# Optimization experiments

Measured on AMD Instinct MI355X. Metric: run time of the kernel, lower is better.

The kernel has to match this reference:

```python
import jax, jax.numpy as jnp
import numpy as np

B, S, D_IN, D_OUT, H = 4, 2048, 1024, 1024, 16
HD = D_OUT // H  # head_dim = 64


def setup_inputs() -> dict:
    key = jax.random.key(0)
    ks = jax.random.split(key, 7)
    sd_in = 1.0 / np.sqrt(D_IN)
    sd_out = 1.0 / np.sqrt(D_OUT)
    return {
        "x": jax.random.normal(ks[0], (B, S, D_IN), dtype=jnp.float32),
        # weights stored [in, out] so y = x @ W (equivalent to torch Linear)
        "wq": jax.random.uniform(ks[1], (D_IN, D_OUT), jnp.float32, -sd_in, sd_in),
        "wk": jax.random.uniform(ks[2], (D_IN, D_OUT), jnp.float32, -sd_in, sd_in),
        "wv": jax.random.uniform(ks[3], (D_IN, D_OUT), jnp.float32, -sd_in, sd_in),
        "wo": jax.random.uniform(ks[4], (D_OUT, D_OUT), jnp.float32, -sd_out, sd_out),
        "bo": jax.random.uniform(ks[5], (D_OUT,), jnp.float32, -sd_out, sd_out),
    }


def reference(x, wq, wk, wv, wo, bo):
    b, n, _ = x.shape
    # project and split heads: [b, h, n, hd]
    q = (x @ wq).reshape(b, n, H, HD).transpose(0, 2, 1, 3)
    k = (x @ wk).reshape(b, n, H, HD).transpose(0, 2, 1, 3)
    v = (x @ wv).reshape(b, n, H, HD).transpose(0, 2, 1, 3)
    scale = 1.0 / jnp.sqrt(jnp.asarray(HD, dtype=x.dtype))
    scores = jnp.einsum('bhqd,bhkd->bhqk', q, k) * scale  # [b,h,n,n]
    causal = jnp.tril(jnp.ones((n, n), dtype=bool))
    scores = jnp.where(causal, scores, -jnp.inf)
    attn = jax.nn.softmax(scores, axis=-1)
    # dropout p=0.0 -> identity
    ctx = jnp.einsum('bhqk,bhkd->bhqd', attn, v)
    ctx = ctx.transpose(0, 2, 1, 3).reshape(b, n, D_OUT)
    return ctx @ wo + bo
```

## Files before the change

kernel.cpp:

```cpp
#include <hip/hip_runtime.h>

#define DEVINL __device__ __forceinline__

typedef __attribute__((ext_vector_type(8))) short s8v;
typedef __attribute__((ext_vector_type(4))) float f4v;
typedef __attribute__((ext_vector_type(16))) float f16v;
typedef __attribute__((ext_vector_type(8))) __bf16 bf8v;
typedef __attribute__((ext_vector_type(4))) unsigned int u4v;

static constexpr int SEQ = 2048;
static constexpr int DIM = 1024;
static constexpr int NH = 16;

DEVINL unsigned short f2bf(float f) {
  unsigned int u = __builtin_bit_cast(unsigned int, f);
  u += 0x7FFFu + ((u >> 16) & 1u);
  return (unsigned short)(u >> 16);
}

DEVINL void gl_lds16(const void* g, void* l) {
  __builtin_amdgcn_global_load_lds((__attribute__((address_space(1))) void*)g,
                                   (__attribute__((address_space(3))) void*)l,
                                   16, 0, 0);
}

DEVINL f4v mfma16(s8v a, s8v b, f4v c) {
  return __builtin_amdgcn_mfma_f32_16x16x32_bf16(__builtin_bit_cast(bf8v, a),
                                                 __builtin_bit_cast(bf8v, b),
                                                 c, 0, 0, 0);
}

DEVINL f16v mfma32(s8v a, s8v b, f16v c) {
  return __builtin_amdgcn_mfma_f32_32x32x16_bf16(__builtin_bit_cast(bf8v, a),
                                                 __builtin_bit_cast(bf8v, b),
                                                 c, 0, 0, 0);
}

DEVINL unsigned cvtpk(float lo, float hi) {
  unsigned r;
  asm("v_cvt_pk_bf16_f32 %0, %1, %2" : "=v"(r) : "v"(lo), "v"(hi));
  return r;
}

DEVINL void plswap(unsigned& a, unsigned& b) {
#if __has_builtin(__builtin_amdgcn_permlane32_swap)
  typedef int i2v __attribute__((ext_vector_type(2)));
  i2v r = __builtin_amdgcn_permlane32_swap((int)a, (int)b, false, false);
  a = (unsigned)r[0]; b = (unsigned)r[1];
#else
  asm volatile("v_permlane32_swap_b32 %0, %1" : "+v"(a), "+v"(b));
#endif
}

DEVINL s8v mkfrag(unsigned w0, unsigned w1, unsigned w2, unsigned w3) {
  u4v t = {w0, w1, w2, w3};
  return __builtin_bit_cast(s8v, t);
}

__global__ __launch_bounds__(256) void k_cvt(const float* __restrict__ in,
                                             unsigned short* __restrict__ outp) {
  const int i = blockIdx.x * 256 + threadIdx.x;
  const f4v* p = (const f4v*)in + (size_t)i * 2;
  f4v a = p[0], b = p[1];
  s8v o;
  o[0] = (short)f2bf(a[0]); o[1] = (short)f2bf(a[1]);
  o[2] = (short)f2bf(a[2]); o[3] = (short)f2bf(a[3]);
  o[4] = (short)f2bf(b[0]); o[5] = (short)f2bf(b[1]);
  o[6] = (short)f2bf(b[2]); o[7] = (short)f2bf(b[3]);
  ((s8v*)outp)[i] = o;
}

__global__ __launch_bounds__(256) void k_twt(const float* __restrict__ w0, const float* __restrict__ w1,
                                             const float* __restrict__ w2, const float* __restrict__ w3,
                                             unsigned short* __restrict__ o0, unsigned short* __restrict__ o1,
                                             unsigned short* __restrict__ o2, unsigned short* __restrict__ o3) {
  __shared__ float tile[32][33];
  const float* w = blockIdx.z == 0 ? w0 : blockIdx.z == 1 ? w1 : blockIdx.z == 2 ? w2 : w3;
  unsigned short* o = blockIdx.z == 0 ? o0 : blockIdx.z == 1 ? o1 : blockIdx.z == 2 ? o2 : o3;
  const int r0 = blockIdx.y * 32, c0 = blockIdx.x * 32;
  const int tx = threadIdx.x & 31, ty = threadIdx.x >> 5;
#pragma unroll
  for (int i = 0; i < 32; i += 8) tile[ty + i][tx] = w[(r0 + ty + i) * DIM + c0 + tx];
  __syncthreads();
#pragma unroll
  for (int i = 0; i < 32; i += 8) o[(c0 + ty + i) * DIM + r0 + tx] = f2bf(tile[tx][ty + i]);
}

static constexpr int SLOT = 49152;
static constexpr int RING_LDS = 147456;

DEVINL void stage_ab(const unsigned short* __restrict__ A, const unsigned short* __restrict__ Bt,
                     int m0, int n0, int k0, char* slot, int tid) {
#pragma unroll
  for (int ld = 0; ld < 2; ++ld) {
    const int c = ld * 512 + tid;
    const int row = c >> 3;
    const int csw = ((c & 7) ^ (row & 7)) * 8;
    gl_lds16(A + (size_t)(m0 + row) * 1024 + k0 + csw, slot + c * 16);
  }
#pragma unroll
  for (int ld = 0; ld < 4; ++ld) {
    const int c = ld * 512 + tid;
    const int row = c >> 3;
    const int csw = ((c & 7) ^ (row & 7)) * 8;
    gl_lds16(Bt + (size_t)(n0 + row) * 1024 + k0 + csw, slot + 16384 + c * 16);
  }
}

DEVINL void gemm_ring3(const unsigned short* __restrict__ A, const unsigned short* __restrict__ Bt,
                       int m0, int n0, char* smem, f4v acc[4][4]) {
  const int tid = threadIdx.x;
  const int lane = tid & 63, l15 = lane & 15, lg = lane >> 4;
  const int wid = tid >> 6, wm = wid >> 2, wn = wid & 3;
  constexpr int NT = 16;

  stage_ab(A, Bt, m0, n0, 0, smem, tid);
  stage_ab(A, Bt, m0, n0, 64, smem + SLOT, tid);

  for (int t = 0; t < NT; ++t) {
    if (t + 2 < NT) {
      stage_ab(A, Bt, m0, n0, (t + 2) * 64, smem + ((t + 2) % 3) * SLOT, tid);
      asm volatile("s_waitcnt vmcnt(12)" ::: "memory");
    } else if (t + 2 == NT) {
      asm volatile("s_waitcnt vmcnt(6)" ::: "memory");
    } else {
      asm volatile("s_waitcnt vmcnt(0)" ::: "memory");
    }
    __builtin_amdgcn_s_barrier();
    __builtin_amdgcn_sched_barrier(0);

    char* Ar = smem + (t % 3) * SLOT;
    char* Br = Ar + 16384;
#pragma unroll
    for (int kk = 0; kk < 2; ++kk) {
      s8v af[4];
#pragma unroll
      for (int mf = 0; mf < 4; ++mf) {
        const int row = wm * 64 + mf * 16 + l15;
        af[mf] = *(const s8v*)(Ar + row * 128 + ((kk * 64 + lg * 16) ^ ((row & 7) << 4)));
      }
#pragma unroll
      for (int nh = 0; nh < 2; ++nh) {
        s8v bfr[2];
#pragma unroll
        for (int j = 0; j < 2; ++j) {
          const int row = wn * 64 + (nh * 2 + j) * 16 + l15;
          bfr[j] = *(const s8v*)(Br + row * 128 + ((kk * 64 + lg * 16) ^ ((row & 7) << 4)));
        }
        __builtin_amdgcn_s_setprio(1);
#pragma unroll
        for (int mf = 0; mf < 4; ++mf) {
          acc[mf][nh * 2 + 0] = mfma16(af[mf], bfr[0], acc[mf][nh * 2 + 0]);
          acc[mf][nh * 2 + 1] = mfma16(af[mf], bfr[1], acc[mf][nh * 2 + 1]);
        }
        __builtin_amdgcn_s_setprio(0);
      }
    }
    __builtin_amdgcn_sched_barrier(0);
    __builtin_amdgcn_s_barrier();
  }
}

__global__ __launch_bounds__(512, 2) void k_qkv(const unsigned short* __restrict__ xb,
                                                const unsigned short* __restrict__ wqt,
                                                const unsigned short* __restrict__ wkt,
                                                const unsigned short* __restrict__ wvt,
                                                unsigned short* __restrict__ q,
                                                unsigned short* __restrict__ k,
                                                unsigned short* __restrict__ v) {
  extern __shared__ __align__(16) char smem[];
  const int wgid = (blockIdx.x & 7) * 96 + (blockIdx.x >> 3);
  const int m0 = (wgid / 12) * 128;
  const int rem = wgid % 12;
  const int which = rem >> 2;
  const int n0 = (rem & 3) * 256;
  const unsigned short* Bt = which == 0 ? wqt : which == 1 ? wkt : wvt;
  unsigned short* C = which == 0 ? q : which == 1 ? k : v;
  const float oscale = which == 0 ? 0.125f * 1.44269504f : 1.0f;
  f4v acc[4][4];
  const f4v z = {0.f, 0.f, 0.f, 0.f};
#pragma unroll
  for (int a = 0; a < 4; ++a)
#pragma unroll
    for (int b = 0; b < 4; ++b) acc[a][b] = z;
  gemm_ring3(xb, Bt, m0, n0, smem, acc);
  const int lane = threadIdx.x & 63, l15 = lane & 15, lg = lane >> 4;
  const int wid = threadIdx.x >> 6, wm = wid >> 2, wn = wid & 3;
#pragma unroll
  for (int mf = 0; mf < 4; ++mf)
#pragma unroll
    for (int nf = 0; nf < 4; ++nf)
#pragma unroll
      for (int r = 0; r < 4; ++r) {
        const int row = m0 + wm * 64 + mf * 16 + lg * 4 + r;
        const int col = n0 + wn * 64 + nf * 16 + l15;
        C[(size_t)row * 1024 + col] = f2bf(acc[mf][nf][r] * oscale);
      }
}

DEVINL void stage128(const unsigned short* __restrict__ A, const unsigned short* __restrict__ Bt,
                     int m0, int n0, int k0, char* Ab, char* Bb, int tid) {
#pragma unroll
  for (int ld = 0; ld < 4; ++ld) {
    const int c = ld * 256 + tid;
    const int row = c >> 3;
    const int csw = ((c & 7) ^ (row & 7)) * 8;
    gl_lds16(A + (size_t)(m0 + row) * 1024 + k0 + csw, Ab + c * 16);
    gl_lds16(Bt + (size_t)(n0 + row) * 1024 + k0 + csw, Bb + c * 16);
  }
}

DEVINL void gemm_compute_tile(char* Ar, char* Br, f4v acc[4][4],
                              int l15, int lg, int wm, int wn) {
#pragma unroll
  for (int kk = 0; kk < 2; ++kk) {
    s8v af[4], bfr[4];
    const int kb2 = (kk * 32 + lg * 8) * 2;
#pragma unroll
    for (int mf = 0; mf < 4; ++mf) {
      const int row = wm * 64 + mf * 16 + l15;
      af[mf] = *(const s8v*)(Ar + row * 128 + (kb2 ^ ((row & 7) << 4)));
    }
#pragma unroll
    for (int nf = 0; nf < 4; ++nf) {
      const int row = wn * 64 + nf * 16 + l15;
      bfr[nf] = *(const s8v*)(Br + row * 128 + (kb2 ^ ((row & 7) << 4)));
    }
#pragma unroll
    for (int mf = 0; mf < 4; ++mf)
#pragma unroll
      for (int nf = 0; nf < 4; ++nf) acc[mf][nf] = mfma16(af[mf], bfr[nf], acc[mf][nf]);
  }
}

DEVINL void gemm_ring2(const unsigned short* __restrict__ A, const unsigned short* __restrict__ Bt,
                       int m0, int n0, char* smem, f4v acc[4][4]) {
  const int tid = threadIdx.x;
  const int lane = tid & 63, l15 = lane & 15, lg = lane >> 4;
  const int wm = (tid >> 6) >> 1, wn = (tid >> 6) & 1;
  constexpr int NT = 16;

  stage128(A, Bt, m0, n0, 0, smem, smem + 32768, tid);

  for (int t = 0; t < NT - 1; ++t) {
    const int nb = (t + 1) & 1;
    stage128(A, Bt, m0, n0, (t + 1) * 64, smem + nb * 16384, smem + 32768 + nb * 16384, tid);
    asm volatile("s_waitcnt vmcnt(8)" ::: "memory");
    __builtin_amdgcn_s_barrier();
    __builtin_amdgcn_sched_barrier(0);
    const int cb = t & 1;
    gemm_compute_tile(smem + cb * 16384, smem + 32768 + cb * 16384, acc, l15, lg, wm, wn);
    asm volatile("s_waitcnt lgkmcnt(0)" ::: "memory");
    __builtin_amdgcn_sched_barrier(0);
    __builtin_amdgcn_s_barrier();
  }
  asm volatile("s_waitcnt vmcnt(0)" ::: "memory");
  __builtin_amdgcn_s_barrier();
  __builtin_amdgcn_sched_barrier(0);
  gemm_compute_tile(smem + ((NT - 1) & 1) * 16384, smem + 32768 + ((NT - 1) & 1) * 16384,
                    acc, l15, lg, wm, wn);
}

__global__ __launch_bounds__(256) void k_oproj(const unsigned short* __restrict__ ctx,
                                               const unsigned short* __restrict__ wot,
                                               const float* __restrict__ bo,
                                               float* __restrict__ outp) {
  __shared__ __align__(16) char smem[65536];
  const int wgid = (blockIdx.x & 7) * 64 + (blockIdx.x >> 3);
  const int m0 = (wgid >> 3) * 128;
  const int n0 = (wgid & 7) * 128;
  f4v acc[4][4];
  const f4v z = {0.f, 0.f, 0.f, 0.f};
#pragma unroll
  for (int a = 0; a < 4; ++a)
#pragma unroll
    for (int b = 0; b < 4; ++b) acc[a][b] = z;
  gemm_ring2(ctx, wot, m0, n0, smem, acc);
  const int lane = threadIdx.x & 63, l15 = lane & 15, lg = lane >> 4;
  const int wm = (threadIdx.x >> 6) >> 1, wn = (threadIdx.x >> 6) & 1;
#pragma unroll
  for (int nf = 0; nf < 4; ++nf) {
    const int col = n0 + wn * 64 + nf * 16 + l15;
    const float bias = bo[col];
#pragma unroll
    for (int mf = 0; mf < 4; ++mf)
#pragma unroll
      for (int r = 0; r < 4; ++r) {
        const int row = m0 + wm * 64 + mf * 16 + lg * 4 + r;
        outp[(size_t)row * 1024 + col] = acc[mf][nf][r] + bias;
      }
  }
}

__global__ __launch_bounds__(256) void k_tv(const unsigned short* __restrict__ v,
                                            unsigned short* __restrict__ vt) {
  __shared__ unsigned short tile[64][65];
  const int b = blockIdx.z, h = blockIdx.y, s0 = blockIdx.x * 64;
  const int t = threadIdx.x;
#pragma unroll
  for (int i = 0; i < 16; ++i) {
    const int s = i * 4 + (t >> 6), d = t & 63;
    tile[s][d] = v[(size_t)(b * SEQ + s0 + s) * 1024 + h * 64 + d];
  }
  __syncthreads();
#pragma unroll
  for (int i = 0; i < 16; ++i) {
    const int d = i * 4 + (t >> 6), s = t & 63;
    vt[(size_t)((b * NH + h) * 64 + d) * SEQ + s0 + s] = tile[s][d];
  }
}

DEVINL void stage_kv(const unsigned short* __restrict__ kbase,
                     const unsigned short* __restrict__ vbase,
                     int kv0, char* Ks, char* Vs, int tid) {
#pragma unroll
  for (int i = 0; i < 2; ++i) {
    const int c = i * 256 + tid;
    const int row = c >> 3;
    const int csw = ((c & 7) ^ (row & 7)) * 8;
    gl_lds16(kbase + (size_t)(kv0 + row) * 1024 + csw, Ks + c * 16);
    gl_lds16(vbase + (size_t)row * SEQ + kv0 + csw, Vs + c * 16);
  }
}

__global__ __launch_bounds__(256) void k_attn(const unsigned short* __restrict__ q,
                                              const unsigned short* __restrict__ kg,
                                              const unsigned short* __restrict__ vt,
                                              unsigned short* __restrict__ ctx) {
  __shared__ __align__(16) char smem[32768];
  const int b = blockIdx.z, h = blockIdx.y, qi = blockIdx.x;
  const int tid = threadIdx.x, lane = tid & 63, w = tid >> 6;
  const int l31 = lane & 31, hi = lane >> 5;

  const unsigned short* kbase = kg + (size_t)b * SEQ * 1024 + h * 64;
  const unsigned short* vbase = vt + (size_t)((b * NH + h) * 64) * SEQ;

  f16v z16;
#pragma unroll
  for (int i = 0; i < 16; ++i) z16[i] = 0.f;

  const int qbb = qi * 128;
  const int qg = qbb + w * 32 + l31;
  const unsigned short* qp = q + (size_t)(b * SEQ + qg) * 1024 + h * 64;
  s8v qf[4];
#pragma unroll
  for (int kd = 0; kd < 4; ++kd) qf[kd] = *(const s8v*)(qp + kd * 16 + hi * 8);

  f16v o0 = z16, o1 = z16;
  float m = -3e38f, lsum = 0.f;
  const int nt = qi * 2 + 2;

  stage_kv(kbase, vbase, 0, smem, smem + 16384, tid);

  for (int t = 0; t < nt; ++t) {
    const int kv0 = t * 64;
    char* Ks = smem + (t & 1) * 8192;
    char* Vs = smem + 16384 + (t & 1) * 8192;
    __syncthreads();
    if (t + 1 < nt)
      stage_kv(kbase, vbase, kv0 + 64, smem + ((t + 1) & 1) * 8192,
               smem + 16384 + ((t + 1) & 1) * 8192, tid);
    if (kv0 > qbb + w * 32 + 31) continue;

    f16v s0 = z16, s1 = z16;
#pragma unroll
    for (int kd = 0; kd < 4; ++kd) {
      const int off = kd * 32 + hi * 16;
      const int r0 = l31, r1 = 32 + l31;
      const s8v kf0 = *(const s8v*)(Ks + r0 * 128 + (off ^ ((r0 & 7) << 4)));
      const s8v kf1 = *(const s8v*)(Ks + r1 * 128 + (off ^ ((r1 & 7) << 4)));
      s0 = mfma32(kf0, qf[kd], s0);
      s1 = mfma32(kf1, qf[kd], s1);
    }

    const bool needmask = (kv0 + 63 > qbb + w * 32);
    const int crel = qg - kv0;
    float tmax = -3e38f;
#pragma unroll
    for (int r = 0; r < 16; ++r) {
      const int kvloc = (r & 3) + 8 * (r >> 2) + 4 * hi;
      float v0 = s0[r], v1 = s1[r];
      if (needmask) {
        if (kvloc > crel) v0 = -3e38f;
        if (kvloc + 32 > crel) v1 = -3e38f;
      }
      s0[r] = v0; s1[r] = v1;
      tmax = fmaxf(tmax, fmaxf(v0, v1));
    }
    tmax = fmaxf(tmax, __shfl_xor(tmax, 32));

    const bool grew = tmax > m + 8.f;
    const float mnew = grew ? tmax : m;
    const float corr = __builtin_amdgcn_exp2f(m - mnew);
    m = mnew;

    float rs = 0.f;
#pragma unroll
    for (int r = 0; r < 16; ++r) {
      const float e0 = __builtin_amdgcn_exp2f(s0[r] - m);
      const float e1 = __builtin_amdgcn_exp2f(s1[r] - m);
      s0[r] = e0; s1[r] = e1;
      rs += e0 + e1;
    }
    rs += __shfl_xor(rs, 32);
    lsum = lsum * corr + rs;
    if (__any(grew)) { o0 *= corr; o1 *= corr; }

    unsigned a0 = cvtpk(s0[0], s0[1]), b0 = cvtpk(s0[4], s0[5]); plswap(a0, b0);
    unsigned a1 = cvtpk(s0[2], s0[3]), b1 = cvtpk(s0[6], s0[7]); plswap(a1, b1);
    const s8v f0 = mkfrag(a0, a1, b0, b1);
    unsigned a2 = cvtpk(s0[8], s0[9]), b2 = cvtpk(s0[12], s0[13]); plswap(a2, b2);
    unsigned a3 = cvtpk(s0[10], s0[11]), b3 = cvtpk(s0[14], s0[15]); plswap(a3, b3);
    const s8v f1 = mkfrag(a2, a3, b2, b3);
    unsigned a4 = cvtpk(s1[0], s1[1]), b4 = cvtpk(s1[4], s1[5]); plswap(a4, b4);
    unsigned a5 = cvtpk(s1[2], s1[3]), b5 = cvtpk(s1[6], s1[7]); plswap(a5, b5);
    const s8v f2 = mkfrag(a4, a5, b4, b5);
    unsigned a6 = cvtpk(s1[8], s1[9]), b6 = cvtpk(s1[12], s1[13]); plswap(a6, b6);
    unsigned a7 = cvtpk(s1[10], s1[11]), b7 = cvtpk(s1[14], s1[15]); plswap(a7, b7);
    const s8v f3 = mkfrag(a6, a7, b6, b7);

#pragma unroll
    for (int ks = 0; ks < 4; ++ks) {
      const s8v pb = ks == 0 ? f0 : ks == 1 ? f1 : ks == 2 ? f2 : f3;
      const int off = ks * 32 + hi * 16;
      const int rd0 = l31, rd1 = 32 + l31;
      const s8v v0 = *(const s8v*)(Vs + rd0 * 128 + (off ^ ((rd0 & 7) << 4)));
      const s8v v1 = *(const s8v*)(Vs + rd1 * 128 + (off ^ ((rd1 & 7) << 4)));
      o0 = mfma32(v0, pb, o0);
      o1 = mfma32(v1, pb, o1);
    }
  }

  const float rl = 1.f / lsum;
  unsigned short* crow_p = ctx + (size_t)(b * SEQ + qg) * 1024 + h * 64;
#pragma unroll
  for (int r = 0; r < 16; ++r) {
    const int d = (r & 3) + 8 * (r >> 2) + 4 * hi;
    crow_p[d] = f2bf(o0[r] * rl);
    crow_p[32 + d] = f2bf(o1[r] * rl);
  }
}

extern "C" void kernel_launch(void* const* d_in, const int* in_sizes, int n_in,
                              void* d_out, int out_size, void* d_ws, size_t ws_size,
                              hipStream_t stream) {
  (void)in_sizes; (void)n_in; (void)out_size; (void)ws_size;
  const float* x = (const float*)d_in[0];
  const float* wq = (const float*)d_in[1];
  const float* wk = (const float*)d_in[2];
  const float* wv = (const float*)d_in[3];
  const float* wo = (const float*)d_in[4];
  const float* bo = (const float*)d_in[5];
  float* outp = (float*)d_out;
  char* ws = (char*)d_ws;
  const size_t MB = 1ull << 20;
  unsigned short* xb  = (unsigned short*)(ws + 0 * MB);
  unsigned short* wqt = (unsigned short*)(ws + 16 * MB);
  unsigned short* wkt = (unsigned short*)(ws + 18 * MB);
  unsigned short* wvt = (unsigned short*)(ws + 20 * MB);
  unsigned short* wot = (unsigned short*)(ws + 22 * MB);
  unsigned short* qb_ = (unsigned short*)(ws + 24 * MB);
  unsigned short* kb_ = (unsigned short*)(ws + 40 * MB);
  unsigned short* vb_ = (unsigned short*)(ws + 56 * MB);
  unsigned short* vtb = (unsigned short*)(ws + 72 * MB);
  unsigned short* ctx = (unsigned short*)(ws + 88 * MB);

  (void)hipFuncSetAttribute((const void*)k_qkv, hipFuncAttributeMaxDynamicSharedMemorySize, RING_LDS);

  k_cvt<<<4096, 256, 0, stream>>>(x, xb);
  k_twt<<<dim3(32, 32, 4), 256, 0, stream>>>(wq, wk, wv, wo, wqt, wkt, wvt, wot);
  k_qkv<<<768, 512, RING_LDS, stream>>>(xb, wqt, wkt, wvt, qb_, kb_, vb_);
  k_tv<<<dim3(32, 16, 4), 256, 0, stream>>>(vb_, vtb);
  k_attn<<<dim3(16, 16, 4), 256, 0, stream>>>(qb_, kb_, vtb, ctx);
  k_oproj<<<512, 256, 0, stream>>>(ctx, wot, bo, outp);
}
```

Baseline: 305.8 us.

## Fuse V transpose into QKV epilogue and pair causal query blocks in attention

The QKV projection epilogue now writes V straight into the transposed [b,h,d,s] layout using 4-element packed stores, which removes the separate k_tv transpose kernel and its round trip through global memory. The attention kernel now processes two query blocks per workgroup (qi and 15-qi), so every workgroup does about the same causal work and the grid is half as large. The costs are scattered 8-byte stores for V with a column-strided pattern, and a serial dependence between the two segments inside each workgroup, which leaves fewer workgroups to hide latency.

```diff
diff --git a/kernel.cpp b/kernel.cpp
--- a/kernel.cpp
+++ b/kernel.cpp
@@ -167,7 +167,7 @@
                                                 const unsigned short* __restrict__ wvt,
                                                 unsigned short* __restrict__ q,
                                                 unsigned short* __restrict__ k,
-                                                unsigned short* __restrict__ v) {
+                                                unsigned short* __restrict__ vt) {
   extern __shared__ __align__(16) char smem[];
   const int wgid = (blockIdx.x & 7) * 96 + (blockIdx.x >> 3);
   const int m0 = (wgid / 12) * 128;
@@ -175,7 +175,6 @@
   const int which = rem >> 2;
   const int n0 = (rem & 3) * 256;
   const unsigned short* Bt = which == 0 ? wqt : which == 1 ? wkt : wvt;
-  unsigned short* C = which == 0 ? q : which == 1 ? k : v;
   const float oscale = which == 0 ? 0.125f * 1.44269504f : 1.0f;
   f4v acc[4][4];
   const f4v z = {0.f, 0.f, 0.f, 0.f};
@@ -186,16 +185,35 @@
   gemm_ring3(xb, Bt, m0, n0, smem, acc);
   const int lane = threadIdx.x & 63, l15 = lane & 15, lg = lane >> 4;
   const int wid = threadIdx.x >> 6, wm = wid >> 2, wn = wid & 3;
-#pragma unroll
-  for (int mf = 0; mf < 4; ++mf)
-#pragma unroll
-    for (int nf = 0; nf < 4; ++nf)
-#pragma unroll
-      for (int r = 0; r < 4; ++r) {
-        const int row = m0 + wm * 64 + mf * 16 + lg * 4 + r;
+  if (which == 2) {
+#pragma unroll
+    for (int mf = 0; mf < 4; ++mf)
+#pragma unroll
+      for (int nf = 0; nf < 4; ++nf) {
+        const int row = m0 + wm * 64 + mf * 16 + lg * 4;
         const int col = n0 + wn * 64 + nf * 16 + l15;
-        C[(size_t)row * 1024 + col] = f2bf(acc[mf][nf][r] * oscale);
-      }
+        const int bb = row >> 11, s = row & 2047;
+        const int h = col >> 6, d = col & 63;
+        ushort4 pk;
+        pk.x = f2bf(acc[mf][nf][0]);
+        pk.y = f2bf(acc[mf][nf][1]);
+        pk.z = f2bf(acc[mf][nf][2]);
+        pk.w = f2bf(acc[mf][nf][3]);
+        *(ushort4*)(vt + ((size_t)((bb * NH + h) * 64 + d) << 11) + s) = pk;
+      }
+  } else {
+    unsigned short* C = which == 0 ? q : k;
+#pragma unroll
+    for (int mf = 0; mf < 4; ++mf)
+#pragma unroll
+      for (int nf = 0; nf < 4; ++nf)
+#pragma unroll
+        for (int r = 0; r < 4; ++r) {
+          const int row = m0 + wm * 64 + mf * 16 + lg * 4 + r;
+          const int col = n0 + wn * 64 + nf * 16 + l15;
+          C[(size_t)row * 1024 + col] = f2bf(acc[mf][nf][r] * oscale);
+        }
+  }
 }
 
 DEVINL void stage128(const unsigned short* __restrict__ A, const unsigned short* __restrict__ Bt,
@@ -292,24 +310,6 @@
   }
 }
 
-__global__ __launch_bounds__(256) void k_tv(const unsigned short* __restrict__ v,
-                                            unsigned short* __restrict__ vt) {
-  __shared__ unsigned short tile[64][65];
-  const int b = blockIdx.z, h = blockIdx.y, s0 = blockIdx.x * 64;
-  const int t = threadIdx.x;
-#pragma unroll
-  for (int i = 0; i < 16; ++i) {
-    const int s = i * 4 + (t >> 6), d = t & 63;
-    tile[s][d] = v[(size_t)(b * SEQ + s0 + s) * 1024 + h * 64 + d];
-  }
-  __syncthreads();
-#pragma unroll
-  for (int i = 0; i < 16; ++i) {
-    const int d = i * 4 + (t >> 6), s = t & 63;
-    vt[(size_t)((b * NH + h) * 64 + d) * SEQ + s0 + s] = tile[s][d];
-  }
-}
-
 DEVINL void stage_kv(const unsigned short* __restrict__ kbase,
                      const unsigned short* __restrict__ vbase,
                      int kv0, char* Ks, char* Vs, int tid) {
@@ -328,7 +328,7 @@
                                               const unsigned short* __restrict__ vt,
                                               unsigned short* __restrict__ ctx) {
   __shared__ __align__(16) char smem[32768];
-  const int b = blockIdx.z, h = blockIdx.y, qi = blockIdx.x;
+  const int b = blockIdx.z, h = blockIdx.y, pair = blockIdx.x;
   const int tid = threadIdx.x, lane = tid & 63, w = tid >> 6;
   const int l31 = lane & 31, hi = lane >> 5;
 
@@ -339,105 +339,109 @@
 #pragma unroll
   for (int i = 0; i < 16; ++i) z16[i] = 0.f;
 
-  const int qbb = qi * 128;
-  const int qg = qbb + w * 32 + l31;
-  const unsigned short* qp = q + (size_t)(b * SEQ + qg) * 1024 + h * 64;
-  s8v qf[4];
-#pragma unroll
-  for (int kd = 0; kd < 4; ++kd) qf[kd] = *(const s8v*)(qp + kd * 16 + hi * 8);
-
-  f16v o0 = z16, o1 = z16;
-  float m = -3e38f, lsum = 0.f;
-  const int nt = qi * 2 + 2;
-
-  stage_kv(kbase, vbase, 0, smem, smem + 16384, tid);
-
-  for (int t = 0; t < nt; ++t) {
-    const int kv0 = t * 64;
-    char* Ks = smem + (t & 1) * 8192;
-    char* Vs = smem + 16384 + (t & 1) * 8192;
+  for (int seg = 0; seg < 2; ++seg) {
+    const int qi = seg == 0 ? pair : 15 - pair;
+    const int qbb = qi * 128;
+    const int qg = qbb + w * 32 + l31;
+    const unsigned short* qp = q + (size_t)(b * SEQ + qg) * 1024 + h * 64;
+    s8v qf[4];
+#pragma unroll
+    for (int kd = 0; kd < 4; ++kd) qf[kd] = *(const s8v*)(qp + kd * 16 + hi * 8);
+
+    f16v o0 = z16, o1 = z16;
+    float m = -3e38f, lsum = 0.f;
+    const int nt = qi * 2 + 2;
+
     __syncthreads();
-    if (t + 1 < nt)
-      stage_kv(kbase, vbase, kv0 + 64, smem + ((t + 1) & 1) * 8192,
-               smem + 16384 + ((t + 1) & 1) * 8192, tid);
-    if (kv0 > qbb + w * 32 + 31) continue;
-
-    f16v s0 = z16, s1 = z16;
-#pragma unroll
-    for (int kd = 0; kd < 4; ++kd) {
-      const int off = kd * 32 + hi * 16;
-      const int r0 = l31, r1 = 32 + l31;
-      const s8v kf0 = *(const s8v*)(Ks + r0 * 128 + (off ^ ((r0 & 7) << 4)));
-      const s8v kf1 = *(const s8v*)(Ks + r1 * 128 + (off ^ ((r1 & 7) << 4)));
-      s0 = mfma32(kf0, qf[kd], s0);
-      s1 = mfma32(kf1, qf[kd], s1);
-    }
-
-    const bool needmask = (kv0 + 63 > qbb + w * 32);
-    const int crel = qg - kv0;
-    float tmax = -3e38f;
+    stage_kv(kbase, vbase, 0, smem, smem + 16384, tid);
+
+    for (int t = 0; t < nt; ++t) {
+      const int kv0 = t * 64;
+      char* Ks = smem + (t & 1) * 8192;
+      char* Vs = smem + 16384 + (t & 1) * 8192;
+      __syncthreads();
+      if (t + 1 < nt)
+        stage_kv(kbase, vbase, kv0 + 64, smem + ((t + 1) & 1) * 8192,
+                 smem + 16384 + ((t + 1) & 1) * 8192, tid);
+      if (kv0 > qbb + w * 32 + 31) continue;
+
+      f16v s0 = z16, s1 = z16;
+#pragma unroll
+      for (int kd = 0; kd < 4; ++kd) {
+        const int off = kd * 32 + hi * 16;
+        const int r0 = l31, r1 = 32 + l31;
+        const s8v kf0 = *(const s8v*)(Ks + r0 * 128 + (off ^ ((r0 & 7) << 4)));
+        const s8v kf1 = *(const s8v*)(Ks + r1 * 128 + (off ^ ((r1 & 7) << 4)));
+        s0 = mfma32(kf0, qf[kd], s0);
+        s1 = mfma32(kf1, qf[kd], s1);
+      }
+
+      const bool needmask = (kv0 + 63 > qbb + w * 32);
+      const int crel = qg - kv0;
+      float tmax = -3e38f;
+#pragma unroll
+      for (int r = 0; r < 16; ++r) {
+        const int kvloc = (r & 3) + 8 * (r >> 2) + 4 * hi;
+        float v0 = s0[r], v1 = s1[r];
+        if (needmask) {
+          if (kvloc > crel) v0 = -3e38f;
+          if (kvloc + 32 > crel) v1 = -3e38f;
+        }
+        s0[r] = v0; s1[r] = v1;
+        tmax = fmaxf(tmax, fmaxf(v0, v1));
+      }
+      tmax = fmaxf(tmax, __shfl_xor(tmax, 32));
+
+      const bool grew = tmax > m + 8.f;
+      const float mnew = grew ? tmax : m;
+      const float corr = __builtin_amdgcn_exp2f(m - mnew);
+      m = mnew;
+
+      float rs = 0.f;
+#pragma unroll
+      for (int r = 0; r < 16; ++r) {
+        const float e0 = __builtin_amdgcn_exp2f(s0[r] - m);
+        const float e1 = __builtin_amdgcn_exp2f(s1[r] - m);
+        s0[r] = e0; s1[r] = e1;
+        rs += e0 + e1;
+      }
+      rs += __shfl_xor(rs, 32);
+      lsum = lsum * corr + rs;
+      if (__any(grew)) { o0 *= corr; o1 *= corr; }
+
+      unsigned a0 = cvtpk(s0[0], s0[1]), b0 = cvtpk(s0[4], s0[5]); plswap(a0, b0);
+      unsigned a1 = cvtpk(s0[2], s0[3]), b1 = cvtpk(s0[6], s0[7]); plswap(a1, b1);
+      const s8v f0 = mkfrag(a0, a1, b0, b1);
+      unsigned a2 = cvtpk(s0[8], s0[9]), b2 = cvtpk(s0[12], s0[13]); plswap(a2, b2);
+      unsigned a3 = cvtpk(s0[10], s0[11]), b3 = cvtpk(s0[14], s0[15]); plswap(a3, b3);
+      const s8v f1 = mkfrag(a2, a3, b2, b3);
+      unsigned a4 = cvtpk(s1[0], s1[1]), b4 = cvtpk(s1[4], s1[5]); plswap(a4, b4);
+      unsigned a5 = cvtpk(s1[2], s1[3]), b5 = cvtpk(s1[6], s1[7]); plswap(a5, b5);
+      const s8v f2 = mkfrag(a4, a5, b4, b5);
+      unsigned a6 = cvtpk(s1[8], s1[9]), b6 = cvtpk(s1[12], s1[13]); plswap(a6, b6);
+      unsigned a7 = cvtpk(s1[10], s1[11]), b7 = cvtpk(s1[14], s1[15]); plswap(a7, b7);
+      const s8v f3 = mkfrag(a6, a7, b6, b7);
+
+#pragma unroll
+      for (int ks = 0; ks < 4; ++ks) {
+        const s8v pb = ks == 0 ? f0 : ks == 1 ? f1 : ks == 2 ? f2 : f3;
+        const int off = ks * 32 + hi * 16;
+        const int rd0 = l31, rd1 = 32 + l31;
+        const s8v v0 = *(const s8v*)(Vs + rd0 * 128 + (off ^ ((rd0 & 7) << 4)));
+        const s8v v1 = *(const s8v*)(Vs + rd1 * 128 + (off ^ ((rd1 & 7) << 4)));
+        o0 = mfma32(v0, pb, o0);
+        o1 = mfma32(v1, pb, o1);
+      }
+    }
+
+    const float rl = 1.f / lsum;
+    unsigned short* crow_p = ctx + (size_t)(b * SEQ + qg) * 1024 + h * 64;
 #pragma unroll
     for (int r = 0; r < 16; ++r) {
-      const int kvloc = (r & 3) + 8 * (r >> 2) + 4 * hi;
-      float v0 = s0[r], v1 = s1[r];
-      if (needmask) {
-        if (kvloc > crel) v0 = -3e38f;
-        if (kvloc + 32 > crel) v1 = -3e38f;
-      }
-      s0[r] = v0; s1[r] = v1;
-      tmax = fmaxf(tmax, fmaxf(v0, v1));
-    }
-    tmax = fmaxf(tmax, __shfl_xor(tmax, 32));
-
-    const bool grew = tmax > m + 8.f;
-    const float mnew = grew ? tmax : m;
-    const float corr = __builtin_amdgcn_exp2f(m - mnew);
-    m = mnew;
-
-    float rs = 0.f;
-#pragma unroll
-    for (int r = 0; r < 16; ++r) {
-      const float e0 = __builtin_amdgcn_exp2f(s0[r] - m);
-      const float e1 = __builtin_amdgcn_exp2f(s1[r] - m);
-      s0[r] = e0; s1[r] = e1;
-      rs += e0 + e1;
-    }
-    rs += __shfl_xor(rs, 32);
-    lsum = lsum * corr + rs;
-    if (__any(grew)) { o0 *= corr; o1 *= corr; }
-
-    unsigned a0 = cvtpk(s0[0], s0[1]), b0 = cvtpk(s0[4], s0[5]); plswap(a0, b0);
-    unsigned a1 = cvtpk(s0[2], s0[3]), b1 = cvtpk(s0[6], s0[7]); plswap(a1, b1);
-    const s8v f0 = mkfrag(a0, a1, b0, b1);
-    unsigned a2 = cvtpk(s0[8], s0[9]), b2 = cvtpk(s0[12], s0[13]); plswap(a2, b2);
-    unsigned a3 = cvtpk(s0[10], s0[11]), b3 = cvtpk(s0[14], s0[15]); plswap(a3, b3);
-    const s8v f1 = mkfrag(a2, a3, b2, b3);
-    unsigned a4 = cvtpk(s1[0], s1[1]), b4 = cvtpk(s1[4], s1[5]); plswap(a4, b4);
-    unsigned a5 = cvtpk(s1[2], s1[3]), b5 = cvtpk(s1[6], s1[7]); plswap(a5, b5);
-    const s8v f2 = mkfrag(a4, a5, b4, b5);
-    unsigned a6 = cvtpk(s1[8], s1[9]), b6 = cvtpk(s1[12], s1[13]); plswap(a6, b6);
-    unsigned a7 = cvtpk(s1[10], s1[11]), b7 = cvtpk(s1[14], s1[15]); plswap(a7, b7);
-    const s8v f3 = mkfrag(a6, a7, b6, b7);
-
-#pragma unroll
-    for (int ks = 0; ks < 4; ++ks) {
-      const s8v pb = ks == 0 ? f0 : ks == 1 ? f1 : ks == 2 ? f2 : f3;
-      const int off = ks * 32 + hi * 16;
-      const int rd0 = l31, rd1 = 32 + l31;
-      const s8v v0 = *(const s8v*)(Vs + rd0 * 128 + (off ^ ((rd0 & 7) << 4)));
-      const s8v v1 = *(const s8v*)(Vs + rd1 * 128 + (off ^ ((rd1 & 7) << 4)));
-      o0 = mfma32(v0, pb, o0);
-      o1 = mfma32(v1, pb, o1);
-    }
-  }
-
-  const float rl = 1.f / lsum;
-  unsigned short* crow_p = ctx + (size_t)(b * SEQ + qg) * 1024 + h * 64;
-#pragma unroll
-  for (int r = 0; r < 16; ++r) {
-    const int d = (r & 3) + 8 * (r >> 2) + 4 * hi;
-    crow_p[d] = f2bf(o0[r] * rl);
-    crow_p[32 + d] = f2bf(o1[r] * rl);
+      const int d = (r & 3) + 8 * (r >> 2) + 4 * hi;
+      crow_p[d] = f2bf(o0[r] * rl);
+      crow_p[32 + d] = f2bf(o1[r] * rl);
+    }
   }
 }
 
@@ -461,7 +465,6 @@
   unsigned short* wot = (unsigned short*)(ws + 22 * MB);
   unsigned short* qb_ = (unsigned short*)(ws + 24 * MB);
   unsigned short* kb_ = (unsigned short*)(ws + 40 * MB);
-  unsigned short* vb_ = (unsigned short*)(ws + 56 * MB);
   unsigned short* vtb = (unsigned short*)(ws + 72 * MB);
   unsigned short* ctx = (unsigned short*)(ws + 88 * MB);
 
@@ -469,8 +472,7 @@
 
   k_cvt<<<4096, 256, 0, stream>>>(x, xb);
   k_twt<<<dim3(32, 32, 4), 256, 0, stream>>>(wq, wk, wv, wo, wqt, wkt, wvt, wot);
-  k_qkv<<<768, 512, RING_LDS, stream>>>(xb, wqt, wkt, wvt, qb_, kb_, vb_);
-  k_tv<<<dim3(32, 16, 4), 256, 0, stream>>>(vb_, vtb);
-  k_attn<<<dim3(16, 16, 4), 256, 0, stream>>>(qb_, kb_, vtb, ctx);
+  k_qkv<<<768, 512, RING_LDS, stream>>>(xb, wqt, wkt, wvt, qb_, kb_, vtb);
+  k_attn<<<dim3(8, 16, 4), 256, 0, stream>>>(qb_, kb_, vtb, ctx);
   k_oproj<<<512, 256, 0, stream>>>(ctx, wot, bo, outp);
 }
```

Measured after the change: 257.3 us. 1.19x faster.
